# Performance work log

Hardware: AMD Instinct MI355X
Metric: run time of the kernel (lower is better)

The kernel has to match this reference:

```python
import jax
jax.config.update("jax_enable_x64", True)
import jax.numpy as jnp
import numpy as np

# Marching-tetrahedra lookup tables (from DMTet.__init__)
TRIANGLE_TABLE = np.array([
    [-1, -1, -1, -1, -1, -1], [1, 0, 2, -1, -1, -1], [4, 0, 3, -1, -1, -1], [1, 4, 2, 1, 3, 4],
    [3, 1, 5, -1, -1, -1], [2, 3, 0, 2, 5, 3], [1, 4, 0, 1, 5, 4], [4, 2, 5, -1, -1, -1],
    [4, 5, 2, -1, -1, -1], [4, 1, 0, 4, 5, 1], [3, 2, 0, 3, 5, 2], [1, 3, 5, -1, -1, -1],
    [4, 1, 2, 4, 3, 1], [3, 0, 4, -1, -1, -1], [2, 0, 1, -1, -1, -1], [-1, -1, -1, -1, -1, -1]],
    dtype=np.int64)
NUM_TRIANGLES_TABLE = np.array([0, 1, 1, 2, 1, 2, 2, 1, 1, 2, 2, 1, 2, 1, 1, 0], dtype=np.int64)
BASE_TET_EDGES = np.array([[0, 1], [0, 2], [0, 3], [1, 2], [1, 3], [2, 3]], dtype=np.int64)


def setup_inputs() -> dict:
    key = jax.random.key(0)
    k1, k2, k3 = jax.random.split(key, 3)
    N, F = 200_000, 1_000_000
    pos_nx3 = jax.random.normal(k1, (N, 3), dtype=jnp.float32)
    sdf_n = jax.random.normal(k2, (N,), dtype=jnp.float32)
    tet_fx4 = jax.random.randint(k3, (F, 4), 0, N).astype(jnp.int64)
    return {"pos_nx3": pos_nx3, "sdf_n": sdf_n, "tet_fx4": tet_fx4}


def reference(pos_nx3, sdf_n, tet_fx4):
    """Marching tetrahedra (DMTet.__call__) with static padded shapes.

    Returns (verts [6F,3], faces [2F,3], vert_valid [6F], face_valid [2F]).
    Padded vert slots are zeros; padded face slots are -1. Valid verts appear
    first, sorted by (min_idx, max_idx) edge key, exactly matching the order
    produced by torch.unique in the original module.
    """
    N = pos_nx3.shape[0]
    Ftet = tet_fx4.shape[0]
    E = Ftet * 6  # upper bound on number of crossing edges
    BIG = jnp.int64(N) * jnp.int64(N)  # sentinel key > any real key

    occ = sdf_n > 0.0                       # [N] bool
    occ_f = occ[tet_fx4]                    # [F,4]
    occ_sum = occ_f.sum(-1)                 # [F]
    valid_tet = (occ_sum > 0) & (occ_sum < 4)

    # all 6 edges per tet, endpoints sorted (sort_edges)
    ev = tet_fx4[:, jnp.asarray(BASE_TET_EDGES)]          # [F,6,2]
    a = jnp.minimum(ev[..., 0], ev[..., 1]).reshape(E)    # [E]
    b = jnp.maximum(ev[..., 0], ev[..., 1]).reshape(E)    # [E]
    keys = a * N + b                                      # unique int64 key per edge
    crossing = occ[a] != occ[b]                           # edge spans the isosurface

    # dedup crossing edges: sort keys (non-crossing pushed to the end), then
    # compact unique sorted keys into the front of a fixed-size buffer
    sortable = jnp.where(crossing, keys, BIG)
    sk = jnp.sort(sortable)                               # [E]
    is_new = jnp.concatenate([jnp.ones((1,), bool), sk[1:] != sk[:-1]])
    rank = jnp.cumsum(is_new) - 1                         # compact slot per sorted entry
    uk = jnp.full((E,), BIG, dtype=jnp.int64).at[rank].set(sk)  # sorted unique keys, BIG-padded
    vert_valid = uk < BIG

    # interpolate surface vertex on each unique crossing edge
    ua = jnp.where(vert_valid, uk // N, 0)
    ub = jnp.where(vert_valid, uk % N, 0)
    sa = sdf_n[ua]
    sb = sdf_n[ub]
    denom = jnp.where(vert_valid, sa - sb, 1.0)
    # torch: verts = pos_a * (-sb/denom) + pos_b * (sa/denom)
    verts = pos_nx3[ua] * (-sb / denom)[:, None] + pos_nx3[ub] * (sa / denom)[:, None]
    verts = jnp.where(vert_valid[:, None], verts, 0.0)

    # map every tet edge to its compact vertex id (-1 if not crossing)
    idx_map = jnp.searchsorted(uk, keys)
    idx_map = jnp.where(crossing, idx_map, -1).reshape(Ftet, 6)

    # triangle-table lookup
    tetindex = (occ_f.astype(jnp.int64) * jnp.array([1, 2, 4, 8], dtype=jnp.int64)).sum(-1)
    tri_tab = jnp.asarray(TRIANGLE_TABLE)[tetindex]       # [F,6]
    ntri = jnp.asarray(NUM_TRIANGLES_TABLE)[tetindex]     # [F]
    face_verts = jnp.take_along_axis(idx_map, jnp.clip(tri_tab, 0, 5), axis=1)  # [F,6]
    m0 = valid_tet & (ntri >= 1)
    m1 = valid_tet & (ntri == 2)
    faces = jnp.concatenate([
        jnp.where(m0[:, None], face_verts[:, :3], -1),
        jnp.where(m1[:, None], face_verts[:, 3:], -1)], axis=0)   # [2F,3]
    face_valid = jnp.concatenate([m0, m1])
    return verts, faces, vert_valid, face_valid
```

## Files before the change

kernel.cpp:

```cpp
#include <hip/hip_runtime.h>

#define SENT 0xFFFFFFFFu
#define BIN_SHIFT 10
#define BIN_W (1 << BIN_SHIFT)
#define MAXBIN 2048
#define CAP 36864
#define VMASK 0x3FFFFu
#define M28 0x0FFFFFFFu
#define DUPBIT 0x80000000u

__constant__ int c_tri[16][6] = {
 {-1,-1,-1,-1,-1,-1},{1,0,2,-1,-1,-1},{4,0,3,-1,-1,-1},{1,4,2,1,3,4},
 {3,1,5,-1,-1,-1},{2,3,0,2,5,3},{1,4,0,1,5,4},{4,2,5,-1,-1,-1},
 {4,5,2,-1,-1,-1},{4,1,0,4,5,1},{3,2,0,3,5,2},{1,3,5,-1,-1,-1},
 {4,1,2,4,3,1},{3,0,4,-1,-1,-1},{2,0,1,-1,-1,-1},{-1,-1,-1,-1,-1,-1}};
__constant__ int c_ntri[16] = {0,1,1,2,1,2,2,1,1,2,2,1,2,1,1,0};
__constant__ int c_ea[6] = {0,0,0,1,1,2};
__constant__ int c_eb[6] = {1,2,3,2,3,3};

__global__ void k_zero_u32(unsigned* p, int n) {
    int i = blockIdx.x * blockDim.x + threadIdx.x;
    int st = gridDim.x * blockDim.x;
    for (; i < n; i += st) p[i] = 0u;
}

__global__ void k_init_cursor(unsigned* gcursor, int nbin) {
    int i = blockIdx.x * blockDim.x + threadIdx.x;
    if (i < nbin) gcursor[i] = (unsigned)i * CAP;
}

__global__ void k_zero_pad(const unsigned* __restrict__ total,
                           float* __restrict__ verts, float* __restrict__ vvalid, int nv) {
    int r = blockIdx.x * blockDim.x + threadIdx.x;
    if (r >= nv) return;
    unsigned V = *total;
    if ((unsigned)r < V) return;
    size_t b = (size_t)r * 3;
    verts[b + 0] = 0.f;
    verts[b + 1] = 0.f;
    verts[b + 2] = 0.f;
    vvalid[r] = 0.f;
}

#define SBS 256
#define SIT 4

__global__ void k_scan1(const unsigned* in, unsigned* out, unsigned* bsum, int n) {
    __shared__ unsigned sm[SBS];
    int t = threadIdx.x, blk = blockIdx.x;
    int base = blk * SBS * SIT + t * SIT;
    unsigned v[SIT];
    unsigned tot = 0;
#pragma unroll
    for (int k = 0; k < SIT; k++) {
        v[k] = (base + k < n) ? in[base + k] : 0u;
        tot += v[k];
    }
    sm[t] = tot;
    __syncthreads();
    for (int off = 1; off < SBS; off <<= 1) {
        unsigned x = (t >= off) ? sm[t - off] : 0u;
        __syncthreads();
        sm[t] += x;
        __syncthreads();
    }
    unsigned run = (t == 0) ? 0u : sm[t - 1];
#pragma unroll
    for (int k = 0; k < SIT; k++) {
        if (base + k < n) out[base + k] = run;
        run += v[k];
    }
    if (t == SBS - 1) bsum[blk] = sm[SBS - 1];
}

__global__ void k_scan2(unsigned* bsum, unsigned* out, int nb, int n) {
    __shared__ unsigned sm[SBS];
    int t = threadIdx.x;
    int k = (nb + SBS - 1) / SBS;
    int st = t * k, en = min(st + k, nb);
    unsigned loc = 0;
    for (int i = st; i < en; i++) loc += bsum[i];
    sm[t] = loc;
    __syncthreads();
    for (int off = 1; off < SBS; off <<= 1) {
        unsigned x = (t >= off) ? sm[t - off] : 0u;
        __syncthreads();
        sm[t] += x;
        __syncthreads();
    }
    unsigned run = (t == 0) ? 0u : sm[t - 1];
    for (int i = st; i < en; i++) {
        unsigned tmp = bsum[i];
        bsum[i] = run;
        run += tmp;
    }
    if (t == SBS - 1) out[n] = run;
}

__global__ void k_scan3(unsigned* out, const unsigned* bsum, int n) {
    int t = threadIdx.x, blk = blockIdx.x;
    int base = blk * SBS * SIT + t * SIT;
    unsigned add = bsum[blk];
#pragma unroll
    for (int k = 0; k < SIT; k++) {
        if (base + k < n) out[base + k] += add;
    }
}

__global__ void k_binscatter2(const int* __restrict__ tet, const float* __restrict__ sdf,
                              unsigned char* __restrict__ tcode,
                              unsigned* __restrict__ gcursor,
                              unsigned* __restrict__ temp_pk,
                              unsigned* __restrict__ eidx, int F, int nbin) {
    __shared__ unsigned s_cnt[MAXBIN];
    __shared__ unsigned s_base[MAXBIN];
    int tid = threadIdx.x;
    for (int i = tid; i < nbin; i += blockDim.x) s_cnt[i] = 0;
    __syncthreads();

    int base = blockIdx.x * (int)blockDim.x * 4;
    int4 tv[4];
    int code[4];
#pragma unroll
    for (int k = 0; k < 4; k++) {
        int f = base + k * (int)blockDim.x + tid;
        code[k] = 0;
        if (f < F) {
            int4 t4 = ((const int4*)tet)[f];
            int c = 0;
            c |= (sdf[t4.x] > 0.f) ? 1 : 0;
            c |= (sdf[t4.y] > 0.f) ? 2 : 0;
            c |= (sdf[t4.z] > 0.f) ? 4 : 0;
            c |= (sdf[t4.w] > 0.f) ? 8 : 0;
            tcode[f] = (unsigned char)c;
            if (c != 0 && c != 15) {
                code[k] = c;
                tv[k] = t4;
            }
        }
    }
#pragma unroll
    for (int k = 0; k < 4; k++) {
        if (!code[k]) continue;
        int v[4] = {tv[k].x, tv[k].y, tv[k].z, tv[k].w};
#pragma unroll
        for (int j = 0; j < 6; j++) {
            int i0 = c_ea[j], i1 = c_eb[j];
            if (((code[k] >> i0) & 1) != ((code[k] >> i1) & 1)) {
                int a = min(v[i0], v[i1]);
                atomicAdd(&s_cnt[a >> BIN_SHIFT], 1u);
            }
        }
    }
    __syncthreads();
    for (int i = tid; i < nbin; i += blockDim.x) {
        unsigned c = s_cnt[i];
        s_base[i] = c ? atomicAdd(&gcursor[i], c) : 0u;
        s_cnt[i] = 0;
    }
    __syncthreads();
#pragma unroll
    for (int k = 0; k < 4; k++) {
        if (!code[k]) continue;
        int f = base + k * (int)blockDim.x + tid;
        int v[4] = {tv[k].x, tv[k].y, tv[k].z, tv[k].w};
#pragma unroll
        for (int j = 0; j < 6; j++) {
            int i0 = c_ea[j], i1 = c_eb[j];
            if (((code[k] >> i0) & 1) != ((code[k] >> i1) & 1)) {
                int a = min(v[i0], v[i1]);
                int b = max(v[i0], v[i1]);
                int bin = a >> BIN_SHIFT;
                unsigned pos = s_base[bin] + atomicAdd(&s_cnt[bin], 1u);
                temp_pk[pos] = ((unsigned)(a & (BIN_W - 1)) << 18) | (unsigned)b;
                eidx[f * 6 + j] = pos;
            }
        }
    }
}

__global__ void k_scan_bins2(const unsigned* __restrict__ gcursor,
                             unsigned* __restrict__ bin_base, int nbin) {
    __shared__ unsigned sm[SBS];
    int t = threadIdx.x;
    int k = (nbin + SBS - 1) / SBS;
    int st = t * k, en = min(st + k, nbin);
    unsigned loc = 0;
    for (int i = st; i < en; i++) loc += gcursor[i] - (unsigned)i * CAP;
    sm[t] = loc;
    __syncthreads();
    for (int off = 1; off < SBS; off <<= 1) {
        unsigned x = (t >= off) ? sm[t - off] : 0u;
        __syncthreads();
        sm[t] += x;
        __syncthreads();
    }
    unsigned run = (t == 0) ? 0u : sm[t - 1];
    for (int i = st; i < en; i++) {
        bin_base[i] = run;
        run += gcursor[i] - (unsigned)i * CAP;
    }
    if (t == SBS - 1) bin_base[nbin] = run;
}

__global__ __launch_bounds__(1024)
void k_fine2(const unsigned* __restrict__ bin_base,
             const unsigned* __restrict__ temp_pk,
             unsigned* __restrict__ pool_b,
             unsigned* __restrict__ tpos,
             unsigned* __restrict__ scat_base, int N, int nbin) {
    __shared__ unsigned s_cnt[BIN_W];
    __shared__ unsigned s_scan[BIN_W];
    int bin = blockIdx.x;
    int tid = threadIdx.x;
    int a0 = bin << BIN_SHIFT;
    int w = min(BIN_W, N - a0);
    unsigned start = bin_base[bin];
    unsigned cnt_bin = bin_base[bin + 1] - start;
    unsigned tstart = (unsigned)bin * CAP;
    s_cnt[tid] = 0;
    __syncthreads();
    for (unsigned i = tid; i < cnt_bin; i += 1024)
        atomicAdd(&s_cnt[temp_pk[tstart + i] >> 18], 1u);
    __syncthreads();
    unsigned c = s_cnt[tid];
    s_scan[tid] = c;
    __syncthreads();
    for (int off = 1; off < BIN_W; off <<= 1) {
        unsigned x = (tid >= off) ? s_scan[tid - off] : 0u;
        __syncthreads();
        s_scan[tid] += x;
        __syncthreads();
    }
    unsigned base = start + s_scan[tid] - c;
    if (tid < w) scat_base[a0 + tid] = base;
    s_cnt[tid] = base;
    if (bin == nbin - 1 && tid == 0) scat_base[N] = bin_base[nbin];
    __syncthreads();
    for (unsigned i = tid; i < cnt_bin; i += 1024) {
        unsigned idx = tstart + i;
        unsigned t = temp_pk[idx];
        unsigned pos = atomicAdd(&s_cnt[t >> 18], 1u);
        pool_b[pos] = t & M28;
        tpos[pos] = idx;
    }
}


__device__ __forceinline__ int find_bin(const unsigned* __restrict__ bin_base,
                                        unsigned idx, int nbin) {
    int lo = 0, hi = nbin - 1;
    while (lo < hi) {
        int mid = (lo + hi + 1) >> 1;
        if (bin_base[mid] <= idx) lo = mid;
        else hi = mid - 1;
    }
    return lo;
}

__global__ void k_markdup(const unsigned* __restrict__ bin_base,
                          const unsigned* __restrict__ scat_base,
                          unsigned* __restrict__ pool_b, int nbin) {
    unsigned total = bin_base[nbin];
    unsigned idx = blockIdx.x * 256u + threadIdx.x;
    if (idx >= total) return;
    int bin = find_bin(bin_base, idx, nbin);
    unsigned p = pool_b[idx];
    unsigned a = ((unsigned)bin << BIN_SHIFT) + (p >> 18);
    unsigned s = scat_base[a];
    bool dup = false;
    for (unsigned j = s; j < idx; j++) {
        if ((pool_b[j] & M28) == p) { dup = true; break; }
    }
    if (dup) pool_b[idx] = p | DUPBIT;
}

__global__ void k_rankem(const unsigned* __restrict__ bin_base,
                         const unsigned* __restrict__ scat_base,
                         const unsigned* __restrict__ pool_b,
                         const unsigned* __restrict__ tpos,
                         unsigned* __restrict__ pool_sorted,
                         unsigned char* __restrict__ rank8,
                         unsigned* __restrict__ cnt, int nbin) {
    unsigned total = bin_base[nbin];
    unsigned idx = blockIdx.x * 256u + threadIdx.x;
    if (idx >= total) return;
    int bin = find_bin(bin_base, idx, nbin);
    unsigned p = pool_b[idx];
    unsigned pm = p & M28;
    unsigned a = ((unsigned)bin << BIN_SHIFT) + (pm >> 18);
    unsigned s = scat_base[a];
    unsigned e = scat_base[a + 1];
    int r = 0;
    for (unsigned j = s; j < e; j++) {
        unsigned q = pool_b[j];
        r += (!(q & DUPBIT) && (q & M28) < pm) ? 1 : 0;
    }
    rank8[tpos[idx]] = (unsigned char)r;
    if (!(p & DUPBIT)) pool_sorted[s + r] = pm & VMASK;
    if (idx == s) {
        int d = 0;
        for (unsigned j = s; j < e; j++) d += (pool_b[j] & DUPBIT) ? 0 : 1;
        cnt[a] = (unsigned)d;
    }
}

__global__ void k_verts(const float* __restrict__ pos, const float* __restrict__ sdf,
                        const unsigned* __restrict__ scat_base, const unsigned* __restrict__ cnt,
                        const unsigned* __restrict__ rank_base, const unsigned* __restrict__ pool_sorted,
                        float* __restrict__ verts, float* __restrict__ vvalid, int N) {
    int a = (int)((blockIdx.x * blockDim.x + threadIdx.x) >> 6);
    int lane = threadIdx.x & 63;
    if (a >= N) return;
    int d = (int)cnt[a];
    if (d == 0) return;
    unsigned s = scat_base[a];
    unsigned rb = rank_base[a];
    float sa = sdf[a];
    float pax = pos[(size_t)a * 3 + 0];
    float pay = pos[(size_t)a * 3 + 1];
    float paz = pos[(size_t)a * 3 + 2];
    for (int i = lane; i < d; i += 64) {
        unsigned b = pool_sorted[s + i];
        float sbv = sdf[b];
        float denom = sa - sbv;
        float w0 = (-sbv) / denom;
        float w1 = sa / denom;
        size_t r = (size_t)(rb + i);
        verts[r * 3 + 0] = pax * w0 + pos[(size_t)b * 3 + 0] * w1;
        verts[r * 3 + 1] = pay * w0 + pos[(size_t)b * 3 + 1] * w1;
        verts[r * 3 + 2] = paz * w0 + pos[(size_t)b * 3 + 2] * w1;
        vvalid[r] = 1.0f;
    }
}

__global__ void k_faces(const int* __restrict__ tet, const unsigned char* __restrict__ tcode,
                        const unsigned* __restrict__ eidx,
                        const unsigned* __restrict__ rank_base,
                        const unsigned char* __restrict__ rank8,
                        float* __restrict__ faces, float* __restrict__ fvalid, int F) {
    int f = blockIdx.x * blockDim.x + threadIdx.x;
    if (f >= F) return;
    int code = tcode[f];
    int nt = c_ntri[code];
    size_t r0 = (size_t)f * 3;
    size_t r1 = ((size_t)F + f) * 3;
    if (nt == 0) {
        faces[r0 + 0] = -1.f; faces[r0 + 1] = -1.f; faces[r0 + 2] = -1.f;
        faces[r1 + 0] = -1.f; faces[r1 + 1] = -1.f; faces[r1 + 2] = -1.f;
        fvalid[f] = 0.f;
        fvalid[F + f] = 0.f;
        return;
    }
    int4 tv = ((const int4*)tet)[f];
    int v[4] = {tv.x, tv.y, tv.z, tv.w};
    float rk[6];
#pragma unroll
    for (int j = 0; j < 6; j++) {
        int i0 = c_ea[j], i1 = c_eb[j];
        if (((code >> i0) & 1) != ((code >> i1) & 1)) {
            int A = min(v[i0], v[i1]);
            rk[j] = (float)(rank_base[A] + (unsigned)rank8[eidx[f * 6 + j]]);
        }
    }
    float f0[3], f1[3] = {-1.f, -1.f, -1.f};
#pragma unroll
    for (int k = 0; k < 3; k++) f0[k] = rk[c_tri[code][k]];
    if (nt == 2) {
#pragma unroll
        for (int k = 0; k < 3; k++) f1[k] = rk[c_tri[code][3 + k]];
    }
    faces[r0 + 0] = f0[0]; faces[r0 + 1] = f0[1]; faces[r0 + 2] = f0[2];
    faces[r1 + 0] = f1[0]; faces[r1 + 1] = f1[1]; faces[r1 + 2] = f1[2];
    fvalid[f] = 1.f;
    fvalid[F + f] = (nt == 2) ? 1.f : 0.f;
}

static void run_scan(const unsigned* in, unsigned* out, unsigned* bsum,
                     int n, hipStream_t stream) {
    int nb = (n + SBS * SIT - 1) / (SBS * SIT);
    k_scan1<<<nb, SBS, 0, stream>>>(in, out, bsum, n);
    k_scan2<<<1, SBS, 0, stream>>>(bsum, out, nb, n);
    k_scan3<<<nb, SBS, 0, stream>>>(out, bsum, n);
}

extern "C" void kernel_launch(void* const* d_in, const int* in_sizes, int n_in,
                              void* d_out, int out_size, void* d_ws, size_t ws_size,
                              hipStream_t stream) {
    const float* pos = (const float*)d_in[0];
    const float* sdf = (const float*)d_in[1];
    const int* tet = (const int*)d_in[2];
    const int N = in_sizes[1];
    const int F = in_sizes[2] / 4;
    const int E = F * 6;
    const int nbin = (N + BIN_W - 1) >> BIN_SHIFT;
    const size_t tempw = (size_t)nbin * CAP;

    float* out = (float*)d_out;
    size_t nverts = (size_t)6 * F;
    size_t nfaces = (size_t)2 * F;
    float* o_verts = out;
    float* o_faces = out + nverts * 3;
    float* o_vvalid = o_faces + nfaces * 3;
    float* o_fvalid = o_vvalid + nverts;

    unsigned* w = (unsigned*)d_ws;
    unsigned* scat_base = w;
    unsigned* cnt = scat_base + N + 1;
    unsigned* rank_base = cnt + N;
    unsigned* bsum = rank_base + N + 1;
    unsigned* bin_base = bsum + 4096;
    unsigned* gcursor = bin_base + MAXBIN + 1;
    unsigned* pool_b = gcursor + MAXBIN;
    unsigned* pool_sorted = pool_b + E;
    unsigned* eidx = pool_sorted + E;
    unsigned* tpos = eidx + E;
    unsigned* temp_pk = tpos + E;
    unsigned char* rank8 = (unsigned char*)(temp_pk + tempw);
    unsigned char* tcode = rank8 + tempw;

    const int BS = 256;
    int gF = (F + BS - 1) / BS;
    int gW = (N + 3) / 4;
    int gE = (E + BS - 1) / BS;
    int gV = (int)((nverts + BS - 1) / BS);
    int gB = (F + BS * 4 - 1) / (BS * 4);

    k_zero_u32<<<(N + BS - 1) / BS, BS, 0, stream>>>(cnt, N);
    k_init_cursor<<<(nbin + BS - 1) / BS, BS, 0, stream>>>(gcursor, nbin);

    k_binscatter2<<<gB, BS, 0, stream>>>(tet, sdf, tcode, gcursor, temp_pk, eidx, F, nbin);

    k_scan_bins2<<<1, SBS, 0, stream>>>(gcursor, bin_base, nbin);

    k_fine2<<<nbin, 1024, 0, stream>>>(bin_base, temp_pk, pool_b, tpos, scat_base, N, nbin);

    k_markdup<<<gE, BS, 0, stream>>>(bin_base, scat_base, pool_b, nbin);
    k_rankem<<<gE, BS, 0, stream>>>(bin_base, scat_base, pool_b, tpos,
                                    pool_sorted, rank8, cnt, nbin);

    run_scan(cnt, rank_base, bsum, N, stream);

    k_zero_pad<<<gV, BS, 0, stream>>>(rank_base + N, o_verts, o_vvalid, (int)nverts);

    k_verts<<<gW, BS, 0, stream>>>(pos, sdf, scat_base, cnt, rank_base, pool_sorted,
                                   o_verts, o_vvalid, N);

    k_faces<<<gF, BS, 0, stream>>>(tet, tcode, eidx, rank_base, rank8,
                                   o_faces, o_fvalid, F);
}
```

Baseline: 342.7 us.

## Fuse duplicate marking and per-vertex count into the fine binning kernel

Moves the duplicate-marking pass and the per-vertex unique count into the per-bin fine scatter kernel. The block reuses its shared-memory scan for segment offsets instead of binary-searching bin_base. This removes the separate markdup kernel, the cnt zeroing kernel, and the count work in k_rankem, cutting launches and global passes. In exchange, the dedup scan now runs inside 1024-thread blocks, one per bin, which may give less parallelism than the per-element launch did. Within a block it relies on a __syncthreads for visibility of global pool_b writes.

```diff
diff --git a/kernel.cpp b/kernel.cpp
--- a/kernel.cpp
+++ b/kernel.cpp
@@ -17,12 +17,6 @@
 __constant__ int c_ntri[16] = {0,1,1,2,1,2,2,1,1,2,2,1,2,1,1,0};
 __constant__ int c_ea[6] = {0,0,0,1,1,2};
 __constant__ int c_eb[6] = {1,2,3,2,3,3};
-
-__global__ void k_zero_u32(unsigned* p, int n) {
-    int i = blockIdx.x * blockDim.x + threadIdx.x;
-    int st = gridDim.x * blockDim.x;
-    for (; i < n; i += st) p[i] = 0u;
-}
 
 __global__ void k_init_cursor(unsigned* gcursor, int nbin) {
     int i = blockIdx.x * blockDim.x + threadIdx.x;
@@ -204,11 +198,12 @@
 }
 
 __global__ __launch_bounds__(1024)
-void k_fine2(const unsigned* __restrict__ bin_base,
+void k_fine3(const unsigned* __restrict__ bin_base,
              const unsigned* __restrict__ temp_pk,
              unsigned* __restrict__ pool_b,
              unsigned* __restrict__ tpos,
-             unsigned* __restrict__ scat_base, int N, int nbin) {
+             unsigned* __restrict__ scat_base,
+             unsigned* __restrict__ cnt, int N, int nbin) {
     __shared__ unsigned s_cnt[BIN_W];
     __shared__ unsigned s_scan[BIN_W];
     int bin = blockIdx.x;
@@ -244,6 +239,26 @@
         pool_b[pos] = t & M28;
         tpos[pos] = idx;
     }
+    __syncthreads();
+    for (unsigned i = tid; i < cnt_bin; i += 1024) {
+        unsigned pp = start + i;
+        unsigned p = pool_b[pp] & M28;
+        unsigned al = p >> 18;
+        unsigned s = start + (al ? s_scan[al - 1] : 0u);
+        bool dup = false;
+        for (unsigned j = s; j < pp; j++) {
+            if ((pool_b[j] & M28) == p) { dup = true; break; }
+        }
+        if (dup) pool_b[pp] = p | DUPBIT;
+    }
+    __syncthreads();
+    if (tid < w) {
+        unsigned s = start + (tid ? s_scan[tid - 1] : 0u);
+        unsigned e = start + s_scan[tid];
+        int d = 0;
+        for (unsigned j = s; j < e; j++) d += (pool_b[j] & DUPBIT) ? 0 : 1;
+        cnt[a0 + tid] = (unsigned)d;
+    }
 }
 
 
@@ -258,30 +273,12 @@
     return lo;
 }
 
-__global__ void k_markdup(const unsigned* __restrict__ bin_base,
-                          const unsigned* __restrict__ scat_base,
-                          unsigned* __restrict__ pool_b, int nbin) {
-    unsigned total = bin_base[nbin];
-    unsigned idx = blockIdx.x * 256u + threadIdx.x;
-    if (idx >= total) return;
-    int bin = find_bin(bin_base, idx, nbin);
-    unsigned p = pool_b[idx];
-    unsigned a = ((unsigned)bin << BIN_SHIFT) + (p >> 18);
-    unsigned s = scat_base[a];
-    bool dup = false;
-    for (unsigned j = s; j < idx; j++) {
-        if ((pool_b[j] & M28) == p) { dup = true; break; }
-    }
-    if (dup) pool_b[idx] = p | DUPBIT;
-}
-
 __global__ void k_rankem(const unsigned* __restrict__ bin_base,
                          const unsigned* __restrict__ scat_base,
                          const unsigned* __restrict__ pool_b,
                          const unsigned* __restrict__ tpos,
                          unsigned* __restrict__ pool_sorted,
-                         unsigned char* __restrict__ rank8,
-                         unsigned* __restrict__ cnt, int nbin) {
+                         unsigned char* __restrict__ rank8, int nbin) {
     unsigned total = bin_base[nbin];
     unsigned idx = blockIdx.x * 256u + threadIdx.x;
     if (idx >= total) return;
@@ -298,11 +295,6 @@
     }
     rank8[tpos[idx]] = (unsigned char)r;
     if (!(p & DUPBIT)) pool_sorted[s + r] = pm & VMASK;
-    if (idx == s) {
-        int d = 0;
-        for (unsigned j = s; j < e; j++) d += (pool_b[j] & DUPBIT) ? 0 : 1;
-        cnt[a] = (unsigned)d;
-    }
 }
 
 __global__ void k_verts(const float* __restrict__ pos, const float* __restrict__ sdf,
@@ -426,18 +418,17 @@
     int gV = (int)((nverts + BS - 1) / BS);
     int gB = (F + BS * 4 - 1) / (BS * 4);
 
-    k_zero_u32<<<(N + BS - 1) / BS, BS, 0, stream>>>(cnt, N);
     k_init_cursor<<<(nbin + BS - 1) / BS, BS, 0, stream>>>(gcursor, nbin);
 
     k_binscatter2<<<gB, BS, 0, stream>>>(tet, sdf, tcode, gcursor, temp_pk, eidx, F, nbin);
 
     k_scan_bins2<<<1, SBS, 0, stream>>>(gcursor, bin_base, nbin);
 
-    k_fine2<<<nbin, 1024, 0, stream>>>(bin_base, temp_pk, pool_b, tpos, scat_base, N, nbin);
-
-    k_markdup<<<gE, BS, 0, stream>>>(bin_base, scat_base, pool_b, nbin);
+    k_fine3<<<nbin, 1024, 0, stream>>>(bin_base, temp_pk, pool_b, tpos,
+                                       scat_base, cnt, N, nbin);
+
     k_rankem<<<gE, BS, 0, stream>>>(bin_base, scat_base, pool_b, tpos,
-                                    pool_sorted, rank8, cnt, nbin);
+                                    pool_sorted, rank8, nbin);
 
     run_scan(cnt, rank_base, bsum, N, stream);
 
```

After: 495.9 us. +44.7%, slower.
